# Kernel optimization log

Hardware: AMD Instinct MI355X
Metric: run time of the kernel (lower is better)

Reference implementation:

```python
import jax, jax.numpy as jnp
import numpy as np

NQ = 64
BIG = 1e10

FILTERS = np.array([[1,0,0,1,0,0,1,0,0],
                    [0,0,0,0,0,0,1,1,1],
                    [0,0,1,0,0,1,0,0,1],
                    [1,1,1,0,0,0,0,0,0],
                    [0,0,0,1,0,0,1,1,0],
                    [0,0,0,0,0,1,0,1,1],
                    [0,1,1,0,0,1,0,0,0],
                    [1,1,0,1,0,0,0,0,0]], dtype=np.float32).reshape(8,1,3,3)


def _conv2d(x, k):
    return jax.lax.conv_general_dilated(x, k, (1,1), 'SAME',
                                        dimension_numbers=('NCHW','OIHW','NCHW'))


def _maxpool3(x):  # 3x3 stride-1 maxpool, pad=1 (pads with -inf like torch)
    return jax.lax.reduce_window(x, -jnp.inf, jax.lax.max, (1,1,3,3), (1,1,1,1), 'SAME')


def setup_inputs() -> dict:
    key = jax.random.key(0)
    ks = jax.random.split(key, 5)
    b, h, w = 2, 240, 320
    n = 2 * h * w  # 153600 points
    fx = fy = 300.0
    cx, cy = w / 2.0, h / 2.0
    z  = jax.random.uniform(ks[0], (b, n), minval=1.0, maxval=10.0)
    u  = jax.random.uniform(ks[1], (b, n), minval=0.0, maxval=float(w))
    v  = jax.random.uniform(ks[2], (b, n), minval=0.0, maxval=float(h))
    xw = (u - cx) / fx * z
    yw = (v - cy) / fy * z
    rgb = jax.random.uniform(ks[3], (b, 3, n))
    pp = jnp.concatenate([xw[:, None], yw[:, None], z[:, None],
                          jnp.ones((b, 1, n), jnp.float32), rgb], axis=1)  # [b,7,n]
    conf = jax.random.uniform(ks[4], (b, n))
    pose_w2c = jnp.tile(jnp.eye(4, dtype=jnp.float32)[None], (b, 1, 1))
    K = jnp.tile(jnp.array([[fx, 0, cx], [0, fy, cy], [0, 0, 1.0]], jnp.float32)[None], (b, 1, 1))
    filters = jnp.asarray(FILTERS)
    return {"pp": pp, "conf": conf, "pose_w2c": pose_w2c, "K": K,
            "filters": filters, "h": h, "w": w}


def reference(pp, conf, pose_w2c, K, filters, h, w,
              znear=0.1, zfar=1000.0, conf_thresh=0.0):
    b, _, n = pp.shape
    # world -> camera (wsz=1 so the hi-res pool is identity)
    pc = jnp.einsum('bij,bjn->bin', pose_w2c, pp[:, :4])          # [b,4,n]
    z  = jnp.abs(pc[:, 2])                                        # [b,n]
    xc = pc[:, 0] * K[:, 0, 0][:, None] / z + K[:, 0, 2][:, None]
    yc = pc[:, 1] * K[:, 1, 1][:, None] / z + K[:, 1, 2][:, None]
    x = jnp.round(xc).astype(jnp.int32)
    y = jnp.round(yc).astype(jnp.int32)
    oob = ((x < 0) | (x >= w) | (y < 0) | (y >= h) |
           (z < znear) | (z > zfar) | (conf <= conf_thresh))
    # inverse-depth quantization bounds over valid points only
    inv_lo = 1.0 / jnp.where(oob, 1e-10, z)   # oob -> 1e10, drops out of min
    inv_hi = 1.0 / jnp.where(oob, BIG, z)     # oob -> 1e-10, drops out of max
    dmin = jnp.min(inv_lo, axis=-1, keepdims=True)
    dmax = jnp.max(inv_hi, axis=-1, keepdims=True)
    do = ((inv_hi - dmin) / (dmax - dmin) * (NQ - 1)).astype(jnp.int32)  # [b,n]

    # scatter points into [b, NQ, h, w] z-buffer bins (drop invalid)
    size = b * NQ * h * w
    bidx = jnp.arange(b, dtype=jnp.int32)[:, None]
    idx = ((bidx * NQ + do) * h + y) * w + x
    idx = jnp.where(oob, size, idx).reshape(-1)   # 'size' is out of bounds -> dropped
    zf = z.astype(jnp.float32).reshape(-1)
    dmap = jnp.zeros((size,), jnp.float32).at[idx].set(zf, mode='drop').reshape(b, NQ, h, w)
    cmap = jnp.full((size,), -1.0, jnp.float32).at[idx].set(conf.reshape(-1), mode='drop').reshape(b, NQ, h, w)
    rgb_pts = pp[:, 4:].transpose(0, 2, 1).reshape(-1, 3).astype(jnp.float32)
    rgb = jnp.zeros((size, 3), jnp.float32).at[idx].set(rgb_pts, mode='drop').reshape(b, NQ, h, w, 3)

    # z-buffer composite: nearest non-empty bin per pixel
    dmap = jnp.where(dmap <= 0, BIG, dmap)
    min_idx = jnp.argmin(dmap, axis=1)                             # [b,h,w]
    dflat = jnp.min(dmap, axis=1)
    dflat = jnp.where(dflat >= BIG, 0.0, dflat)
    cflat = jnp.take_along_axis(cmap, min_idx[:, None], axis=1)[:, 0]
    cflat = jnp.maximum(cflat, 0.0)                                # cmap_[cmap_<0]=0
    rflat = jnp.take_along_axis(rgb, min_idx[:, None, :, :, None], axis=1)[:, 0]  # [b,h,w,3]

    # vertical flip (torch.flip over h)
    depths = dflat[:, ::-1][:, None]                               # [b,1,h,w]
    confs  = cflat[:, ::-1][:, None]
    rgbs   = jnp.transpose(rflat[:, ::-1], (0, 3, 1, 2))           # [b,3,h,w]

    # hole filling: 2 iterations of oriented-filter tests + 3x3 max pooling
    ones_k = jnp.ones((1, 1, 3, 3), jnp.float32)
    for _ in range(2):
        tofill = (_conv2d(depths, ones_k) > 0) & (depths <= 0)
        o = _conv2d(depths, filters)                               # [b,8,h,w]
        fill = (jnp.abs(jnp.prod(o, axis=1, keepdims=True)) > 1e-10) & tofill
        f = fill.astype(jnp.float32)
        depths = depths * (1 - f) + f * _maxpool3(depths)
        confs  = confs  * (1 - f) + f * _maxpool3(confs)
        rgbs   = rgbs   * (1 - f) + f * _maxpool3(rgbs)
    return depths, confs, rgbs
```

## Files before the change

kernel.cpp:

```cpp
#include <hip/hip_runtime.h>
#include <stdint.h>

#define NQ 64
#define ZNEAR 0.1f
#define ZFAR 1000.0f
#define FT 16

__device__ __forceinline__ float wave_min_f(float v) {
    #pragma unroll
    for (int off = 1; off < 64; off <<= 1)
        v = fminf(v, __shfl_xor(v, off, 64));
    return v;
}
__device__ __forceinline__ float wave_max_f(float v) {
    #pragma unroll
    for (int off = 1; off < 64; off <<= 1)
        v = fmaxf(v, __shfl_xor(v, off, 64));
    return v;
}

__global__ void k_project(const float* __restrict__ pp, const float* __restrict__ conf,
                          const float* __restrict__ pose, const float* __restrict__ Km,
                          const int* __restrict__ hp, const int* __restrict__ wp,
                          int B, int n,
                          float* __restrict__ zbuf, unsigned* __restrict__ packed,
                          float4* __restrict__ cr4,
                          float* __restrict__ pmin, float* __restrict__ pmax, int nBlk,
                          unsigned* __restrict__ pixwin, int pixTot) {
    int bb = blockIdx.y;
    int i = blockIdx.x * blockDim.x + threadIdx.x;
    size_t ztid = ((size_t)blockIdx.y * gridDim.x + blockIdx.x) * blockDim.x + threadIdx.x;
    if (ztid < (size_t)pixTot) pixwin[ztid] = 0u;

    int h = *hp, w = *wp;
    float inv_lo = INFINITY;
    float inv_hi = 0.0f;
    if (i < n) {
        const float* P  = pose + (size_t)bb * 16;
        const float* km = Km   + (size_t)bb * 9;
        const float* pb = pp   + (size_t)bb * 7 * n;
        float X  = pb[0 * (size_t)n + i];
        float Y  = pb[1 * (size_t)n + i];
        float Z  = pb[2 * (size_t)n + i];
        float Wc = pb[3 * (size_t)n + i];
        float pc0 = P[0] * X + P[1] * Y + P[2]  * Z + P[3]  * Wc;
        float pc1 = P[4] * X + P[5] * Y + P[6]  * Z + P[7]  * Wc;
        float pc2 = P[8] * X + P[9] * Y + P[10] * Z + P[11] * Wc;
        float z = fabsf(pc2);
        float xc = pc0 * km[0] / z + km[2];
        float yc = pc1 * km[4] / z + km[5];
        float xr = rintf(xc);
        float yr = rintf(yc);
        float cf = conf[(size_t)bb * n + i];
        bool valid = (xr >= 0.0f) && (xr <= (float)(w - 1)) &&
                     (yr >= 0.0f) && (yr <= (float)(h - 1)) &&
                     (z >= ZNEAR) && (z <= ZFAR) && (cf > 0.0f);
        unsigned px = valid ? (unsigned)(int)xr : 0u;
        unsigned py = valid ? (unsigned)(int)yr : 0u;
        size_t p = (size_t)bb * n + i;
        zbuf[p] = z;
        packed[p] = (valid ? 0x80000000u : 0u) | px | (py << 12);
        cr4[p] = make_float4(cf, pb[4 * (size_t)n + i], pb[5 * (size_t)n + i], pb[6 * (size_t)n + i]);
        inv_lo = valid ? (1.0f / z) : (1.0f / 1e-10f);
        inv_hi = valid ? (1.0f / z) : (1.0f / 1e10f);
    }
    __shared__ float smin[4], smax[4];
    float wmin = wave_min_f(inv_lo);
    float wmax = wave_max_f(inv_hi);
    int lane = threadIdx.x & 63, wid = threadIdx.x >> 6;
    if (lane == 0) { smin[wid] = wmin; smax[wid] = wmax; }
    __syncthreads();
    if (threadIdx.x == 0) {
        pmin[(size_t)bb * nBlk + blockIdx.x] = fminf(fminf(smin[0], smin[1]), fminf(smin[2], smin[3]));
        pmax[(size_t)bb * nBlk + blockIdx.x] = fmaxf(fmaxf(smax[0], smax[1]), fmaxf(smax[2], smax[3]));
    }
}

__global__ void k_scatter(const float* __restrict__ zbuf, const unsigned* __restrict__ packed,
                          const float* __restrict__ pminb, const float* __restrict__ pmaxb, int nBlk,
                          const int* __restrict__ hp, const int* __restrict__ wp,
                          int B, int n, unsigned* __restrict__ pixwin) {
    __shared__ float smin[4], smax[4];
    __shared__ float sdlo[8], sdhi[8];
    for (int bb = 0; bb < B; ++bb) {
        float lmin = INFINITY, lmax = 0.0f;
        for (int k = threadIdx.x; k < nBlk; k += blockDim.x) {
            lmin = fminf(lmin, pminb[(size_t)bb * nBlk + k]);
            lmax = fmaxf(lmax, pmaxb[(size_t)bb * nBlk + k]);
        }
        lmin = wave_min_f(lmin);
        lmax = wave_max_f(lmax);
        int lane = threadIdx.x & 63, wid = threadIdx.x >> 6;
        if (lane == 0) { smin[wid] = lmin; smax[wid] = lmax; }
        __syncthreads();
        if (threadIdx.x == 0) {
            sdlo[bb] = fminf(fminf(smin[0], smin[1]), fminf(smin[2], smin[3]));
            sdhi[bb] = fmaxf(fmaxf(smax[0], smax[1]), fmaxf(smax[2], smax[3]));
        }
        __syncthreads();
    }
    int p = blockIdx.x * blockDim.x + threadIdx.x;
    if (p >= B * n) return;
    unsigned pk = packed[p];
    if (!(pk & 0x80000000u)) return;
    int bb = p / n;
    int i = p - bb * n;
    float inv = 1.0f / zbuf[p];
    float dlo = sdlo[bb], dhi = sdhi[bb];
    int dq = (int)((inv - dlo) / (dhi - dlo) * (float)(NQ - 1));
    int h = *hp, w = *wp;
    int x = (int)(pk & 0xFFFu);
    int y = (int)((pk >> 12) & 0xFFFu);
    unsigned key = ((unsigned)dq << 20) | (unsigned)(i + 1);
    atomicMax(&pixwin[(size_t)bb * h * w + (size_t)y * w + x], key);
}

__global__ void k_resfill(const float* __restrict__ zbuf, const float4* __restrict__ cr4,
                          const unsigned* __restrict__ pixwin,
                          const float* __restrict__ filt,
                          const int* __restrict__ hp, const int* __restrict__ wp,
                          int B, int n, float* __restrict__ out, int pixTot) {
    int h = *hp, w = *wp;
    int tilesX = (w + FT - 1) / FT;
    int tilesY = (h + FT - 1) / FT;
    int tile = blockIdx.x;
    if (tile >= tilesX * tilesY) return;
    int bb = blockIdx.y;
    int tY = tile / tilesX, tX = tile - tY * tilesX;
    int gy0 = tY * FT - 2, gx0 = tX * FT - 2;
    int hw = h * w;

    __shared__ float s_f[72];
    __shared__ float s_in[5][20][20];
    __shared__ float s_m[5][18][18];
    int tid = threadIdx.x;
    if (tid < 72) s_f[tid] = filt[tid];

    for (int idx = tid; idx < 400; idx += blockDim.x) {
        int yy = idx / 20, xx = idx - yy * 20;
        int gy = gy0 + yy, gx = gx0 + xx;
        float v0 = 0.0f, v1 = 0.0f, v2 = 0.0f, v3 = 0.0f, v4 = 0.0f;
        if (((unsigned)gy < (unsigned)h) && ((unsigned)gx < (unsigned)w)) {
            int ys = h - 1 - gy;
            unsigned key = pixwin[(size_t)bb * hw + (size_t)ys * w + gx];
            if (key) {
                int i = (int)(key & 0xFFFFFu) - 1;
                size_t p = (size_t)bb * n + i;
                v0 = zbuf[p];
                float4 cr = cr4[p];
                v1 = cr.x; v2 = cr.y; v3 = cr.z; v4 = cr.w;
            }
        }
        s_in[0][yy][xx] = v0;
        s_in[1][yy][xx] = v1;
        s_in[2][yy][xx] = v2;
        s_in[3][yy][xx] = v3;
        s_in[4][yy][xx] = v4;
    }
    __syncthreads();

    for (int idx = tid; idx < 324; idx += blockDim.x) {
        int py = idx / 18, px = idx - py * 18;
        int sy = py + 1, sx = px + 1;
        int gy = gy0 + sy, gx = gx0 + sx;
        bool vc = ((unsigned)gy < (unsigned)h) && ((unsigned)gx < (unsigned)w);
        float d[9];
        #pragma unroll
        for (int t = 0; t < 9; ++t) d[t] = s_in[0][sy + t / 3 - 1][sx + t % 3 - 1];
        float s = 0.0f;
        #pragma unroll
        for (int t = 0; t < 9; ++t) s += d[t];
        float dc0 = d[4];
        float ov[5];
        #pragma unroll
        for (int ch = 0; ch < 5; ++ch) ov[ch] = s_in[ch][sy][sx];
        if ((s > 0.0f) && (dc0 <= 0.0f)) {
            float prod = 1.0f;
            #pragma unroll
            for (int k = 0; k < 8; ++k) {
                float o = 0.0f;
                #pragma unroll
                for (int t = 0; t < 9; ++t) o += s_f[k * 9 + t] * d[t];
                prod *= o;
            }
            if (fabsf(prod) > 1e-10f) {
                #pragma unroll
                for (int ch = 0; ch < 5; ++ch) {
                    float m = -INFINITY;
                    #pragma unroll
                    for (int t = 0; t < 9; ++t) {
                        int ny = gy + t / 3 - 1, nx = gx + t % 3 - 1;
                        if (((unsigned)ny < (unsigned)h) && ((unsigned)nx < (unsigned)w))
                            m = fmaxf(m, s_in[ch][sy + t / 3 - 1][sx + t % 3 - 1]);
                    }
                    ov[ch] = m;
                }
            }
        }
        if (!vc) { ov[0] = 0.0f; ov[1] = 0.0f; ov[2] = 0.0f; ov[3] = 0.0f; ov[4] = 0.0f; }
        #pragma unroll
        for (int ch = 0; ch < 5; ++ch) s_m[ch][py][px] = ov[ch];
    }
    __syncthreads();

    int ly = tid >> 4, lx = tid & 15;
    int gy = tY * FT + ly, gx = tX * FT + lx;
    if (((unsigned)gy < (unsigned)h) && ((unsigned)gx < (unsigned)w)) {
        int sy = ly + 1, sx = lx + 1;
        float d[9];
        #pragma unroll
        for (int t = 0; t < 9; ++t) d[t] = s_m[0][sy + t / 3 - 1][sx + t % 3 - 1];
        float s = 0.0f;
        #pragma unroll
        for (int t = 0; t < 9; ++t) s += d[t];
        float dc0 = d[4];
        float ov[5];
        #pragma unroll
        for (int ch = 0; ch < 5; ++ch) ov[ch] = s_m[ch][sy][sx];
        if ((s > 0.0f) && (dc0 <= 0.0f)) {
            float prod = 1.0f;
            #pragma unroll
            for (int k = 0; k < 8; ++k) {
                float o = 0.0f;
                #pragma unroll
                for (int t = 0; t < 9; ++t) o += s_f[k * 9 + t] * d[t];
                prod *= o;
            }
            if (fabsf(prod) > 1e-10f) {
                #pragma unroll
                for (int ch = 0; ch < 5; ++ch) {
                    float m = -INFINITY;
                    #pragma unroll
                    for (int t = 0; t < 9; ++t) {
                        int ny = gy + t / 3 - 1, nx = gx + t % 3 - 1;
                        if (((unsigned)ny < (unsigned)h) && ((unsigned)nx < (unsigned)w))
                            m = fmaxf(m, s_m[ch][sy + t / 3 - 1][sx + t % 3 - 1]);
                    }
                    ov[ch] = m;
                }
            }
        }
        size_t g = (size_t)gy * w + gx;
        out[(size_t)bb * hw + g] = ov[0];
        out[(size_t)pixTot + (size_t)bb * hw + g] = ov[1];
        size_t rb = 2 * (size_t)pixTot;
        out[rb + (((size_t)bb * 3 + 0) * hw) + g] = ov[2];
        out[rb + (((size_t)bb * 3 + 1) * hw) + g] = ov[3];
        out[rb + (((size_t)bb * 3 + 2) * hw) + g] = ov[4];
    }
}

static inline size_t align16(size_t x) { return (x + 15) & ~(size_t)15; }

extern "C" void kernel_launch(void* const* d_in, const int* in_sizes, int n_in,
                              void* d_out, int out_size, void* d_ws, size_t ws_size,
                              hipStream_t stream) {
    const float* pp   = (const float*)d_in[0];
    const float* conf = (const float*)d_in[1];
    const float* pose = (const float*)d_in[2];
    const float* Km   = (const float*)d_in[3];
    const float* filt = (const float*)d_in[4];
    const int*   hp   = (const int*)d_in[5];
    const int*   wp   = (const int*)d_in[6];

    int B = in_sizes[2] / 16;
    int n = in_sizes[1] / B;
    size_t pix = (size_t)out_size / 5;
    size_t npts = (size_t)B * n;
    size_t hw = pix / B;

    const int bs = 256;
    int nBlk = (n + bs - 1) / bs;

    char* ws = (char*)d_ws;
    size_t off = 0;
    unsigned* pixwin = (unsigned*)(ws + off);  off = align16(off + pix * 4);
    float* zbuf   = (float*)(ws + off);        off = align16(off + npts * 4);
    unsigned* packed = (unsigned*)(ws + off);  off = align16(off + npts * 4);
    float4* cr4   = (float4*)(ws + off);       off = align16(off + npts * 16);
    float* pminb  = (float*)(ws + off);        off = align16(off + (size_t)B * nBlk * 4);
    float* pmaxb  = (float*)(ws + off);        off = align16(off + (size_t)B * nBlk * 4);

    float* out = (float*)d_out;
    int pixI = (int)pix;

    dim3 gproj(nBlk, B);
    k_project<<<gproj, bs, 0, stream>>>(pp, conf, pose, Km, hp, wp, B, n,
                                        zbuf, packed, cr4, pminb, pmaxb, nBlk,
                                        pixwin, pixI);

    int nptsI = (int)npts;
    k_scatter<<<(nptsI + bs - 1) / bs, bs, 0, stream>>>(zbuf, packed, pminb, pmaxb, nBlk,
                                                        hp, wp, B, n, pixwin);

    size_t tileBound = hw / (FT * FT) + hw / FT + 2;
    dim3 gfill((unsigned)tileBound, B);
    k_resfill<<<gfill, bs, 0, stream>>>(zbuf, cr4, pixwin, filt, hp, wp, B, n, out, pixI);
}
```

Measured before the change: 105.5 us.

## Fuse projection, scatter and hole-fill into one cooperative persistent kernel

Replaces the three-kernel pipeline (project, scatter, resfill) with a single cooperative kernel that uses grid.sync between phases. Per-batch depth min/max is reduced across blocks in-kernel using unsigned-float atomics in shared memory, and the grid is sized from occupancy times CU count. This removes two kernel launch gaps and the separate reduction, at the cost of grid-wide barriers and a persistent grid that may under-occupy each phase. If the cooperative launch fails, it falls back to the old path.

```diff
diff --git a/kernel.cpp b/kernel.cpp
--- a/kernel.cpp
+++ b/kernel.cpp
@@ -1,10 +1,15 @@
 #include <hip/hip_runtime.h>
+#include <hip/hip_cooperative_groups.h>
 #include <stdint.h>
+
+namespace cg = cooperative_groups;
 
 #define NQ 64
 #define ZNEAR 0.1f
 #define ZFAR 1000.0f
 #define FT 16
+#define BMAX 8
+#define GMAX 2048
 
 __device__ __forceinline__ float wave_min_f(float v) {
     #pragma unroll
@@ -17,6 +22,277 @@
     for (int off = 1; off < 64; off <<= 1)
         v = fmaxf(v, __shfl_xor(v, off, 64));
     return v;
+}
+__device__ __forceinline__ unsigned wave_umin_u(unsigned v) {
+    #pragma unroll
+    for (int off = 1; off < 64; off <<= 1) {
+        unsigned o = (unsigned)__shfl_xor((int)v, off, 64);
+        v = (v < o) ? v : o;
+    }
+    return v;
+}
+__device__ __forceinline__ unsigned wave_umax_u(unsigned v) {
+    #pragma unroll
+    for (int off = 1; off < 64; off <<= 1) {
+        unsigned o = (unsigned)__shfl_xor((int)v, off, 64);
+        v = (v > o) ? v : o;
+    }
+    return v;
+}
+
+__global__ void __launch_bounds__(256, 4)
+k_fused(const float* __restrict__ pp, const float* __restrict__ conf,
+        const float* __restrict__ pose, const float* __restrict__ Km,
+        const float* __restrict__ filt,
+        const int* __restrict__ hp, const int* __restrict__ wp,
+        int B, int n,
+        float* __restrict__ zbuf, unsigned* __restrict__ packed,
+        float4* __restrict__ cr4,
+        unsigned* __restrict__ pminU, unsigned* __restrict__ pmaxU,
+        unsigned* __restrict__ pixwin, float* __restrict__ out)
+{
+    cg::grid_group grid = cg::this_grid();
+    const int h = *hp, w = *wp;
+    const int hw = h * w;
+    const int pixTot = B * hw;
+    const int npts = B * n;
+    const int tid = (int)threadIdx.x;
+    const int gsz = (int)(gridDim.x * blockDim.x);
+    const int gtid = (int)(blockIdx.x * blockDim.x) + tid;
+
+    __shared__ unsigned bmn[BMAX], bmx[BMAX];
+    __shared__ unsigned fw[8];
+    __shared__ float sdlo[BMAX], sdhi[BMAX];
+    __shared__ float s_f[72];
+    __shared__ float s_in[5][20][20];
+    __shared__ float s_m[5][18][18];
+
+    if (tid < BMAX) { bmn[tid] = 0xFFFFFFFFu; bmx[tid] = 0u; }
+    if (tid < 72) s_f[tid] = filt[tid];
+    __syncthreads();
+
+    for (int idx = gtid; idx < pixTot; idx += gsz) pixwin[idx] = 0u;
+
+    int iters = (npts + gsz - 1) / gsz;
+    for (int it = 0; it < iters; ++it) {
+        int p = gtid + it * gsz;
+        bool act = p < npts;
+        int pc = act ? p : (npts - 1);
+        int bb = pc / n;
+        int i = pc - bb * n;
+        unsigned ulo = 0xFFFFFFFFu, uhi = 0u;
+        if (act) {
+            const float* P  = pose + (size_t)bb * 16;
+            const float* km = Km   + (size_t)bb * 9;
+            const float* pb = pp   + (size_t)bb * 7 * n;
+            float X  = pb[0 * (size_t)n + i];
+            float Y  = pb[1 * (size_t)n + i];
+            float Z  = pb[2 * (size_t)n + i];
+            float Wc = pb[3 * (size_t)n + i];
+            float pc0 = P[0] * X + P[1] * Y + P[2]  * Z + P[3]  * Wc;
+            float pc1 = P[4] * X + P[5] * Y + P[6]  * Z + P[7]  * Wc;
+            float pc2 = P[8] * X + P[9] * Y + P[10] * Z + P[11] * Wc;
+            float z = fabsf(pc2);
+            float xc = pc0 * km[0] / z + km[2];
+            float yc = pc1 * km[4] / z + km[5];
+            float xr = rintf(xc);
+            float yr = rintf(yc);
+            float cf = conf[p];
+            bool valid = (xr >= 0.0f) && (xr <= (float)(w - 1)) &&
+                         (yr >= 0.0f) && (yr <= (float)(h - 1)) &&
+                         (z >= ZNEAR) && (z <= ZFAR) && (cf > 0.0f);
+            unsigned px = valid ? (unsigned)(int)xr : 0u;
+            unsigned py = valid ? (unsigned)(int)yr : 0u;
+            zbuf[p] = z;
+            packed[p] = (valid ? 0x80000000u : 0u) | px | (py << 12);
+            cr4[p] = make_float4(cf, pb[4 * (size_t)n + i], pb[5 * (size_t)n + i], pb[6 * (size_t)n + i]);
+            float ilo = valid ? (1.0f / z) : (1.0f / 1e-10f);
+            float ihi = valid ? (1.0f / z) : (1.0f / 1e10f);
+            ulo = __float_as_uint(ilo);
+            uhi = __float_as_uint(ihi);
+        }
+        int bb0 = __shfl(bb, 0, 64);
+        if (__all(bb == bb0)) {
+            unsigned wl = wave_umin_u(ulo);
+            unsigned wh = wave_umax_u(uhi);
+            if ((tid & 63) == 0) { atomicMin(&bmn[bb0], wl); atomicMax(&bmx[bb0], wh); }
+        } else if (act) {
+            atomicMin(&bmn[bb], ulo);
+            atomicMax(&bmx[bb], uhi);
+        }
+    }
+    __syncthreads();
+    if (tid < B) {
+        pminU[(size_t)tid * gridDim.x + blockIdx.x] = bmn[tid];
+        pmaxU[(size_t)tid * gridDim.x + blockIdx.x] = bmx[tid];
+    }
+
+    grid.sync();
+
+    for (int bb = 0; bb < B; ++bb) {
+        unsigned lmin = 0xFFFFFFFFu, lmax = 0u;
+        for (int k = tid; k < (int)gridDim.x; k += (int)blockDim.x) {
+            unsigned a  = pminU[(size_t)bb * gridDim.x + k];
+            unsigned b2 = pmaxU[(size_t)bb * gridDim.x + k];
+            lmin = (lmin < a)  ? lmin : a;
+            lmax = (lmax > b2) ? lmax : b2;
+        }
+        lmin = wave_umin_u(lmin);
+        lmax = wave_umax_u(lmax);
+        int lane = tid & 63, wid = tid >> 6;
+        if (lane == 0) { fw[wid] = lmin; fw[4 + wid] = lmax; }
+        __syncthreads();
+        if (tid == 0) {
+            unsigned m0 = fw[0]; m0 = (m0 < fw[1]) ? m0 : fw[1];
+            m0 = (m0 < fw[2]) ? m0 : fw[2]; m0 = (m0 < fw[3]) ? m0 : fw[3];
+            unsigned m1 = fw[4]; m1 = (m1 > fw[5]) ? m1 : fw[5];
+            m1 = (m1 > fw[6]) ? m1 : fw[6]; m1 = (m1 > fw[7]) ? m1 : fw[7];
+            sdlo[bb] = __uint_as_float(m0);
+            sdhi[bb] = __uint_as_float(m1);
+        }
+        __syncthreads();
+    }
+
+    for (int p = gtid; p < npts; p += gsz) {
+        unsigned pk = packed[p];
+        if (!(pk & 0x80000000u)) continue;
+        int bb = p / n;
+        int i = p - bb * n;
+        float inv = 1.0f / zbuf[p];
+        float dlo = sdlo[bb], dhi = sdhi[bb];
+        int dq = (int)((inv - dlo) / (dhi - dlo) * (float)(NQ - 1));
+        int x = (int)(pk & 0xFFFu);
+        int y = (int)((pk >> 12) & 0xFFFu);
+        unsigned key = ((unsigned)dq << 20) | (unsigned)(i + 1);
+        atomicMax(&pixwin[(size_t)bb * hw + (size_t)y * w + x], key);
+    }
+
+    grid.sync();
+
+    int tilesX = (w + FT - 1) / FT;
+    int tilesY = (h + FT - 1) / FT;
+    int tpb = tilesX * tilesY;
+    int totTiles = B * tpb;
+    for (int t = (int)blockIdx.x; t < totTiles; t += (int)gridDim.x) {
+        int bb = t / tpb;
+        int tile = t - bb * tpb;
+        int tY = tile / tilesX, tX = tile - tY * tilesX;
+        int gy0 = tY * FT - 2, gx0 = tX * FT - 2;
+
+        for (int idx = tid; idx < 400; idx += (int)blockDim.x) {
+            int yy = idx / 20, xx = idx - yy * 20;
+            int gy = gy0 + yy, gx = gx0 + xx;
+            float v0 = 0.0f, v1 = 0.0f, v2 = 0.0f, v3 = 0.0f, v4 = 0.0f;
+            if (((unsigned)gy < (unsigned)h) && ((unsigned)gx < (unsigned)w)) {
+                int ys = h - 1 - gy;
+                unsigned key = pixwin[(size_t)bb * hw + (size_t)ys * w + gx];
+                if (key) {
+                    int i = (int)(key & 0xFFFFFu) - 1;
+                    size_t p = (size_t)bb * n + i;
+                    v0 = zbuf[p];
+                    float4 cr = cr4[p];
+                    v1 = cr.x; v2 = cr.y; v3 = cr.z; v4 = cr.w;
+                }
+            }
+            s_in[0][yy][xx] = v0;
+            s_in[1][yy][xx] = v1;
+            s_in[2][yy][xx] = v2;
+            s_in[3][yy][xx] = v3;
+            s_in[4][yy][xx] = v4;
+        }
+        __syncthreads();
+
+        for (int idx = tid; idx < 324; idx += (int)blockDim.x) {
+            int py = idx / 18, px = idx - py * 18;
+            int sy = py + 1, sx = px + 1;
+            int gy = gy0 + sy, gx = gx0 + sx;
+            bool vc = ((unsigned)gy < (unsigned)h) && ((unsigned)gx < (unsigned)w);
+            float d[9];
+            #pragma unroll
+            for (int tt = 0; tt < 9; ++tt) d[tt] = s_in[0][sy + tt / 3 - 1][sx + tt % 3 - 1];
+            float s = 0.0f;
+            #pragma unroll
+            for (int tt = 0; tt < 9; ++tt) s += d[tt];
+            float dc0 = d[4];
+            float ov[5];
+            #pragma unroll
+            for (int ch = 0; ch < 5; ++ch) ov[ch] = s_in[ch][sy][sx];
+            if ((s > 0.0f) && (dc0 <= 0.0f)) {
+                float prod = 1.0f;
+                #pragma unroll
+                for (int k = 0; k < 8; ++k) {
+                    float o = 0.0f;
+                    #pragma unroll
+                    for (int tt = 0; tt < 9; ++tt) o += s_f[k * 9 + tt] * d[tt];
+                    prod *= o;
+                }
+                if (fabsf(prod) > 1e-10f) {
+                    #pragma unroll
+                    for (int ch = 0; ch < 5; ++ch) {
+                        float m = -INFINITY;
+                        #pragma unroll
+                        for (int tt = 0; tt < 9; ++tt) {
+                            int ny = gy + tt / 3 - 1, nx = gx + tt % 3 - 1;
+                            if (((unsigned)ny < (unsigned)h) && ((unsigned)nx < (unsigned)w))
+                                m = fmaxf(m, s_in[ch][sy + tt / 3 - 1][sx + tt % 3 - 1]);
+                        }
+                        ov[ch] = m;
+                    }
+                }
+            }
+            if (!vc) { ov[0] = 0.0f; ov[1] = 0.0f; ov[2] = 0.0f; ov[3] = 0.0f; ov[4] = 0.0f; }
+            #pragma unroll
+            for (int ch = 0; ch < 5; ++ch) s_m[ch][py][px] = ov[ch];
+        }
+        __syncthreads();
+
+        int ly = tid >> 4, lx = tid & 15;
+        int gy = tY * FT + ly, gx = tX * FT + lx;
+        if (((unsigned)gy < (unsigned)h) && ((unsigned)gx < (unsigned)w)) {
+            int sy = ly + 1, sx = lx + 1;
+            float d[9];
+            #pragma unroll
+            for (int tt = 0; tt < 9; ++tt) d[tt] = s_m[0][sy + tt / 3 - 1][sx + tt % 3 - 1];
+            float s = 0.0f;
+            #pragma unroll
+            for (int tt = 0; tt < 9; ++tt) s += d[tt];
+            float dc0 = d[4];
+            float ov[5];
+            #pragma unroll
+            for (int ch = 0; ch < 5; ++ch) ov[ch] = s_m[ch][sy][sx];
+            if ((s > 0.0f) && (dc0 <= 0.0f)) {
+                float prod = 1.0f;
+                #pragma unroll
+                for (int k = 0; k < 8; ++k) {
+                    float o = 0.0f;
+                    #pragma unroll
+                    for (int tt = 0; tt < 9; ++tt) o += s_f[k * 9 + tt] * d[tt];
+                    prod *= o;
+                }
+                if (fabsf(prod) > 1e-10f) {
+                    #pragma unroll
+                    for (int ch = 0; ch < 5; ++ch) {
+                        float m = -INFINITY;
+                        #pragma unroll
+                        for (int tt = 0; tt < 9; ++tt) {
+                            int ny = gy + tt / 3 - 1, nx = gx + tt % 3 - 1;
+                            if (((unsigned)ny < (unsigned)h) && ((unsigned)nx < (unsigned)w))
+                                m = fmaxf(m, s_m[ch][sy + tt / 3 - 1][sx + tt % 3 - 1]);
+                        }
+                        ov[ch] = m;
+                    }
+                }
+            }
+            size_t g = (size_t)gy * w + gx;
+            out[(size_t)bb * hw + g] = ov[0];
+            out[(size_t)pixTot + (size_t)bb * hw + g] = ov[1];
+            size_t rb = 2 * (size_t)pixTot;
+            out[rb + (((size_t)bb * 3 + 0) * hw) + g] = ov[2];
+            out[rb + (((size_t)bb * 3 + 1) * hw) + g] = ov[3];
+            out[rb + (((size_t)bb * 3 + 2) * hw) + g] = ov[4];
+        }
+        __syncthreads();
+    }
 }
 
 __global__ void k_project(const float* __restrict__ pp, const float* __restrict__ conf,
@@ -267,7 +543,6 @@
     int n = in_sizes[1] / B;
     size_t pix = (size_t)out_size / 5;
     size_t npts = (size_t)B * n;
-    size_t hw = pix / B;
 
     const int bs = 256;
     int nBlk = (n + bs - 1) / bs;
@@ -278,11 +553,41 @@
     float* zbuf   = (float*)(ws + off);        off = align16(off + npts * 4);
     unsigned* packed = (unsigned*)(ws + off);  off = align16(off + npts * 4);
     float4* cr4   = (float4*)(ws + off);       off = align16(off + npts * 16);
-    float* pminb  = (float*)(ws + off);        off = align16(off + (size_t)B * nBlk * 4);
-    float* pmaxb  = (float*)(ws + off);        off = align16(off + (size_t)B * nBlk * 4);
+    unsigned* pminU = (unsigned*)(ws + off);   off = align16(off + (size_t)GMAX * BMAX * 4);
+    unsigned* pmaxU = (unsigned*)(ws + off);   off = align16(off + (size_t)GMAX * BMAX * 4);
 
     float* out = (float*)d_out;
     int pixI = (int)pix;
+
+    static int G = 0;
+    if (G == 0) {
+        int nb = 0;
+        if (hipOccupancyMaxActiveBlocksPerMultiprocessor(&nb, k_fused, bs, 0) != hipSuccess || nb < 1)
+            nb = 2;
+        int dev = 0;
+        hipGetDevice(&dev);
+        int cus = 0;
+        if (hipDeviceGetAttribute(&cus, hipDeviceAttributeMultiprocessorCount, dev) != hipSuccess || cus < 1)
+            cus = 256;
+        long long g = (long long)nb * cus;
+        if (g > GMAX) g = GMAX;
+        if (g < 64) g = 64;
+        G = (int)g;
+    }
+
+    {
+        void* kargs[] = { (void*)&pp, (void*)&conf, (void*)&pose, (void*)&Km, (void*)&filt,
+                          (void*)&hp, (void*)&wp, (void*)&B, (void*)&n,
+                          (void*)&zbuf, (void*)&packed, (void*)&cr4,
+                          (void*)&pminU, (void*)&pmaxU, (void*)&pixwin, (void*)&out };
+        hipError_t e = hipLaunchCooperativeKernel((const void*)k_fused, dim3((unsigned)G), dim3(bs),
+                                                  kargs, 0, stream);
+        if (e == hipSuccess) return;
+    }
+
+    float* pminb = (float*)pminU;
+    float* pmaxb = (float*)pmaxU;
+    size_t hw = pix / B;
 
     dim3 gproj(nBlk, B);
     k_project<<<gproj, bs, 0, stream>>>(pp, conf, pose, Km, hp, wp, B, n,
```

After: 225.8 us. 2.14x slower.

## Pack depth into 64-bit winner key and grid-stride fill tiles

Applied to the files above, without the earlier changes.

The per-pixel winner key becomes 64 bits, with the point's depth bits in the low word, so the fill kernel reads depth straight from the key instead of gathering from zbuf. Projection writes a single interleaved uint2 (packed coords plus z) in place of two separate arrays, and the scatter kernel does one 8-byte load. The fill kernel changes from one block per tile with a loose tile bound to a persistent grid-stride loop over tiles with a capped grid. In exchange the atomics and the pixel buffer double in width, and each tile iteration now needs an extra barrier.

```diff
diff --git a/kernel.cpp b/kernel.cpp
--- a/kernel.cpp
+++ b/kernel.cpp
@@ -23,14 +23,13 @@
                           const float* __restrict__ pose, const float* __restrict__ Km,
                           const int* __restrict__ hp, const int* __restrict__ wp,
                           int B, int n,
-                          float* __restrict__ zbuf, unsigned* __restrict__ packed,
-                          float4* __restrict__ cr4,
+                          uint2* __restrict__ pz, float4* __restrict__ cr4,
                           float* __restrict__ pmin, float* __restrict__ pmax, int nBlk,
-                          unsigned* __restrict__ pixwin, int pixTot) {
+                          unsigned long long* __restrict__ pixwin, int pixTot) {
     int bb = blockIdx.y;
     int i = blockIdx.x * blockDim.x + threadIdx.x;
     size_t ztid = ((size_t)blockIdx.y * gridDim.x + blockIdx.x) * blockDim.x + threadIdx.x;
-    if (ztid < (size_t)pixTot) pixwin[ztid] = 0u;
+    if (ztid < (size_t)pixTot) pixwin[ztid] = 0ull;
 
     int h = *hp, w = *wp;
     float inv_lo = INFINITY;
@@ -58,8 +57,7 @@
         unsigned px = valid ? (unsigned)(int)xr : 0u;
         unsigned py = valid ? (unsigned)(int)yr : 0u;
         size_t p = (size_t)bb * n + i;
-        zbuf[p] = z;
-        packed[p] = (valid ? 0x80000000u : 0u) | px | (py << 12);
+        pz[p] = make_uint2((valid ? 0x80000000u : 0u) | px | (py << 12), __float_as_uint(z));
         cr4[p] = make_float4(cf, pb[4 * (size_t)n + i], pb[5 * (size_t)n + i], pb[6 * (size_t)n + i]);
         inv_lo = valid ? (1.0f / z) : (1.0f / 1e-10f);
         inv_hi = valid ? (1.0f / z) : (1.0f / 1e10f);
@@ -76,10 +74,10 @@
     }
 }
 
-__global__ void k_scatter(const float* __restrict__ zbuf, const unsigned* __restrict__ packed,
+__global__ void k_scatter(const uint2* __restrict__ pz,
                           const float* __restrict__ pminb, const float* __restrict__ pmaxb, int nBlk,
                           const int* __restrict__ hp, const int* __restrict__ wp,
-                          int B, int n, unsigned* __restrict__ pixwin) {
+                          int B, int n, unsigned long long* __restrict__ pixwin) {
     __shared__ float smin[4], smax[4];
     __shared__ float sdlo[8], sdhi[8];
     for (int bb = 0; bb < B; ++bb) {
@@ -101,152 +99,160 @@
     }
     int p = blockIdx.x * blockDim.x + threadIdx.x;
     if (p >= B * n) return;
-    unsigned pk = packed[p];
+    uint2 v = pz[p];
+    unsigned pk = v.x;
     if (!(pk & 0x80000000u)) return;
     int bb = p / n;
     int i = p - bb * n;
-    float inv = 1.0f / zbuf[p];
+    float z = __uint_as_float(v.y);
+    float inv = 1.0f / z;
     float dlo = sdlo[bb], dhi = sdhi[bb];
     int dq = (int)((inv - dlo) / (dhi - dlo) * (float)(NQ - 1));
     int h = *hp, w = *wp;
     int x = (int)(pk & 0xFFFu);
     int y = (int)((pk >> 12) & 0xFFFu);
-    unsigned key = ((unsigned)dq << 20) | (unsigned)(i + 1);
+    unsigned key32 = ((unsigned)dq << 20) | (unsigned)(i + 1);
+    unsigned long long key = ((unsigned long long)key32 << 32) | (unsigned long long)v.y;
     atomicMax(&pixwin[(size_t)bb * h * w + (size_t)y * w + x], key);
 }
 
-__global__ void k_resfill(const float* __restrict__ zbuf, const float4* __restrict__ cr4,
-                          const unsigned* __restrict__ pixwin,
+__global__ void k_resfill(const float4* __restrict__ cr4,
+                          const unsigned long long* __restrict__ pixwin,
                           const float* __restrict__ filt,
                           const int* __restrict__ hp, const int* __restrict__ wp,
                           int B, int n, float* __restrict__ out, int pixTot) {
     int h = *hp, w = *wp;
+    int hw = h * w;
     int tilesX = (w + FT - 1) / FT;
     int tilesY = (h + FT - 1) / FT;
-    int tile = blockIdx.x;
-    if (tile >= tilesX * tilesY) return;
-    int bb = blockIdx.y;
-    int tY = tile / tilesX, tX = tile - tY * tilesX;
-    int gy0 = tY * FT - 2, gx0 = tX * FT - 2;
-    int hw = h * w;
+    int tpb = tilesX * tilesY;
+    int totTiles = B * tpb;
+    int tid = threadIdx.x;
 
     __shared__ float s_f[72];
     __shared__ float s_in[5][20][20];
     __shared__ float s_m[5][18][18];
-    int tid = threadIdx.x;
     if (tid < 72) s_f[tid] = filt[tid];
 
-    for (int idx = tid; idx < 400; idx += blockDim.x) {
-        int yy = idx / 20, xx = idx - yy * 20;
-        int gy = gy0 + yy, gx = gx0 + xx;
-        float v0 = 0.0f, v1 = 0.0f, v2 = 0.0f, v3 = 0.0f, v4 = 0.0f;
+    for (int t = (int)blockIdx.x; t < totTiles; t += (int)gridDim.x) {
+        int bb = t / tpb;
+        int tile = t - bb * tpb;
+        int tY = tile / tilesX, tX = tile - tY * tilesX;
+        int gy0 = tY * FT - 2, gx0 = tX * FT - 2;
+
+        for (int idx = tid; idx < 400; idx += (int)blockDim.x) {
+            int yy = idx / 20, xx = idx - yy * 20;
+            int gy = gy0 + yy, gx = gx0 + xx;
+            float v0 = 0.0f, v1 = 0.0f, v2 = 0.0f, v3 = 0.0f, v4 = 0.0f;
+            if (((unsigned)gy < (unsigned)h) && ((unsigned)gx < (unsigned)w)) {
+                int ys = h - 1 - gy;
+                unsigned long long key = pixwin[(size_t)bb * hw + (size_t)ys * w + gx];
+                if (key) {
+                    int i = (int)((unsigned)(key >> 32) & 0xFFFFFu) - 1;
+                    size_t p = (size_t)bb * n + i;
+                    v0 = __uint_as_float((unsigned)(key & 0xFFFFFFFFull));
+                    float4 cr = cr4[p];
+                    v1 = cr.x; v2 = cr.y; v3 = cr.z; v4 = cr.w;
+                }
+            }
+            s_in[0][yy][xx] = v0;
+            s_in[1][yy][xx] = v1;
+            s_in[2][yy][xx] = v2;
+            s_in[3][yy][xx] = v3;
+            s_in[4][yy][xx] = v4;
+        }
+        __syncthreads();
+
+        for (int idx = tid; idx < 324; idx += (int)blockDim.x) {
+            int py = idx / 18, px = idx - py * 18;
+            int sy = py + 1, sx = px + 1;
+            int gy = gy0 + sy, gx = gx0 + sx;
+            bool vc = ((unsigned)gy < (unsigned)h) && ((unsigned)gx < (unsigned)w);
+            float d[9];
+            #pragma unroll
+            for (int tt = 0; tt < 9; ++tt) d[tt] = s_in[0][sy + tt / 3 - 1][sx + tt % 3 - 1];
+            float s = 0.0f;
+            #pragma unroll
+            for (int tt = 0; tt < 9; ++tt) s += d[tt];
+            float dc0 = d[4];
+            float ov[5];
+            #pragma unroll
+            for (int ch = 0; ch < 5; ++ch) ov[ch] = s_in[ch][sy][sx];
+            if ((s > 0.0f) && (dc0 <= 0.0f)) {
+                float prod = 1.0f;
+                #pragma unroll
+                for (int k = 0; k < 8; ++k) {
+                    float o = 0.0f;
+                    #pragma unroll
+                    for (int tt = 0; tt < 9; ++tt) o += s_f[k * 9 + tt] * d[tt];
+                    prod *= o;
+                }
+                if (fabsf(prod) > 1e-10f) {
+                    #pragma unroll
+                    for (int ch = 0; ch < 5; ++ch) {
+                        float m = -INFINITY;
+                        #pragma unroll
+                        for (int tt = 0; tt < 9; ++tt) {
+                            int ny = gy + tt / 3 - 1, nx = gx + tt % 3 - 1;
+                            if (((unsigned)ny < (unsigned)h) && ((unsigned)nx < (unsigned)w))
+                                m = fmaxf(m, s_in[ch][sy + tt / 3 - 1][sx + tt % 3 - 1]);
+                        }
+                        ov[ch] = m;
+                    }
+                }
+            }
+            if (!vc) { ov[0] = 0.0f; ov[1] = 0.0f; ov[2] = 0.0f; ov[3] = 0.0f; ov[4] = 0.0f; }
+            #pragma unroll
+            for (int ch = 0; ch < 5; ++ch) s_m[ch][py][px] = ov[ch];
+        }
+        __syncthreads();
+
+        int ly = tid >> 4, lx = tid & 15;
+        int gy = tY * FT + ly, gx = tX * FT + lx;
         if (((unsigned)gy < (unsigned)h) && ((unsigned)gx < (unsigned)w)) {
-            int ys = h - 1 - gy;
-            unsigned key = pixwin[(size_t)bb * hw + (size_t)ys * w + gx];
-            if (key) {
-                int i = (int)(key & 0xFFFFFu) - 1;
-                size_t p = (size_t)bb * n + i;
-                v0 = zbuf[p];
-                float4 cr = cr4[p];
-                v1 = cr.x; v2 = cr.y; v3 = cr.z; v4 = cr.w;
+            int sy = ly + 1, sx = lx + 1;
+            float d[9];
+            #pragma unroll
+            for (int tt = 0; tt < 9; ++tt) d[tt] = s_m[0][sy + tt / 3 - 1][sx + tt % 3 - 1];
+            float s = 0.0f;
+            #pragma unroll
+            for (int tt = 0; tt < 9; ++tt) s += d[tt];
+            float dc0 = d[4];
+            float ov[5];
+            #pragma unroll
+            for (int ch = 0; ch < 5; ++ch) ov[ch] = s_m[ch][sy][sx];
+            if ((s > 0.0f) && (dc0 <= 0.0f)) {
+                float prod = 1.0f;
+                #pragma unroll
+                for (int k = 0; k < 8; ++k) {
+                    float o = 0.0f;
+                    #pragma unroll
+                    for (int tt = 0; tt < 9; ++tt) o += s_f[k * 9 + tt] * d[tt];
+                    prod *= o;
+                }
+                if (fabsf(prod) > 1e-10f) {
+                    #pragma unroll
+                    for (int ch = 0; ch < 5; ++ch) {
+                        float m = -INFINITY;
+                        #pragma unroll
+                        for (int tt = 0; tt < 9; ++tt) {
+                            int ny = gy + tt / 3 - 1, nx = gx + tt % 3 - 1;
+                            if (((unsigned)ny < (unsigned)h) && ((unsigned)nx < (unsigned)w))
+                                m = fmaxf(m, s_m[ch][sy + tt / 3 - 1][sx + tt % 3 - 1]);
+                        }
+                        ov[ch] = m;
+                    }
+                }
             }
-        }
-        s_in[0][yy][xx] = v0;
-        s_in[1][yy][xx] = v1;
-        s_in[2][yy][xx] = v2;
-        s_in[3][yy][xx] = v3;
-        s_in[4][yy][xx] = v4;
-    }
-    __syncthreads();
-
-    for (int idx = tid; idx < 324; idx += blockDim.x) {
-        int py = idx / 18, px = idx - py * 18;
-        int sy = py + 1, sx = px + 1;
-        int gy = gy0 + sy, gx = gx0 + sx;
-        bool vc = ((unsigned)gy < (unsigned)h) && ((unsigned)gx < (unsigned)w);
-        float d[9];
-        #pragma unroll
-        for (int t = 0; t < 9; ++t) d[t] = s_in[0][sy + t / 3 - 1][sx + t % 3 - 1];
-        float s = 0.0f;
-        #pragma unroll
-        for (int t = 0; t < 9; ++t) s += d[t];
-        float dc0 = d[4];
-        float ov[5];
-        #pragma unroll
-        for (int ch = 0; ch < 5; ++ch) ov[ch] = s_in[ch][sy][sx];
-        if ((s > 0.0f) && (dc0 <= 0.0f)) {
-            float prod = 1.0f;
-            #pragma unroll
-            for (int k = 0; k < 8; ++k) {
-                float o = 0.0f;
-                #pragma unroll
-                for (int t = 0; t < 9; ++t) o += s_f[k * 9 + t] * d[t];
-                prod *= o;
-            }
-            if (fabsf(prod) > 1e-10f) {
-                #pragma unroll
-                for (int ch = 0; ch < 5; ++ch) {
-                    float m = -INFINITY;
-                    #pragma unroll
-                    for (int t = 0; t < 9; ++t) {
-                        int ny = gy + t / 3 - 1, nx = gx + t % 3 - 1;
-                        if (((unsigned)ny < (unsigned)h) && ((unsigned)nx < (unsigned)w))
-                            m = fmaxf(m, s_in[ch][sy + t / 3 - 1][sx + t % 3 - 1]);
-                    }
-                    ov[ch] = m;
-                }
-            }
-        }
-        if (!vc) { ov[0] = 0.0f; ov[1] = 0.0f; ov[2] = 0.0f; ov[3] = 0.0f; ov[4] = 0.0f; }
-        #pragma unroll
-        for (int ch = 0; ch < 5; ++ch) s_m[ch][py][px] = ov[ch];
-    }
-    __syncthreads();
-
-    int ly = tid >> 4, lx = tid & 15;
-    int gy = tY * FT + ly, gx = tX * FT + lx;
-    if (((unsigned)gy < (unsigned)h) && ((unsigned)gx < (unsigned)w)) {
-        int sy = ly + 1, sx = lx + 1;
-        float d[9];
-        #pragma unroll
-        for (int t = 0; t < 9; ++t) d[t] = s_m[0][sy + t / 3 - 1][sx + t % 3 - 1];
-        float s = 0.0f;
-        #pragma unroll
-        for (int t = 0; t < 9; ++t) s += d[t];
-        float dc0 = d[4];
-        float ov[5];
-        #pragma unroll
-        for (int ch = 0; ch < 5; ++ch) ov[ch] = s_m[ch][sy][sx];
-        if ((s > 0.0f) && (dc0 <= 0.0f)) {
-            float prod = 1.0f;
-            #pragma unroll
-            for (int k = 0; k < 8; ++k) {
-                float o = 0.0f;
-                #pragma unroll
-                for (int t = 0; t < 9; ++t) o += s_f[k * 9 + t] * d[t];
-                prod *= o;
-            }
-            if (fabsf(prod) > 1e-10f) {
-                #pragma unroll
-                for (int ch = 0; ch < 5; ++ch) {
-                    float m = -INFINITY;
-                    #pragma unroll
-                    for (int t = 0; t < 9; ++t) {
-                        int ny = gy + t / 3 - 1, nx = gx + t % 3 - 1;
-                        if (((unsigned)ny < (unsigned)h) && ((unsigned)nx < (unsigned)w))
-                            m = fmaxf(m, s_m[ch][sy + t / 3 - 1][sx + t % 3 - 1]);
-                    }
-                    ov[ch] = m;
-                }
-            }
-        }
-        size_t g = (size_t)gy * w + gx;
-        out[(size_t)bb * hw + g] = ov[0];
-        out[(size_t)pixTot + (size_t)bb * hw + g] = ov[1];
-        size_t rb = 2 * (size_t)pixTot;
-        out[rb + (((size_t)bb * 3 + 0) * hw) + g] = ov[2];
-        out[rb + (((size_t)bb * 3 + 1) * hw) + g] = ov[3];
-        out[rb + (((size_t)bb * 3 + 2) * hw) + g] = ov[4];
+            size_t g = (size_t)gy * w + gx;
+            out[(size_t)bb * hw + g] = ov[0];
+            out[(size_t)pixTot + (size_t)bb * hw + g] = ov[1];
+            size_t rb = 2 * (size_t)pixTot;
+            out[rb + (((size_t)bb * 3 + 0) * hw) + g] = ov[2];
+            out[rb + (((size_t)bb * 3 + 1) * hw) + g] = ov[3];
+            out[rb + (((size_t)bb * 3 + 2) * hw) + g] = ov[4];
+        }
+        __syncthreads();
     }
 }
 
@@ -274,9 +280,8 @@
 
     char* ws = (char*)d_ws;
     size_t off = 0;
-    unsigned* pixwin = (unsigned*)(ws + off);  off = align16(off + pix * 4);
-    float* zbuf   = (float*)(ws + off);        off = align16(off + npts * 4);
-    unsigned* packed = (unsigned*)(ws + off);  off = align16(off + npts * 4);
+    unsigned long long* pixwin = (unsigned long long*)(ws + off);  off = align16(off + pix * 8);
+    uint2* pz     = (uint2*)(ws + off);        off = align16(off + npts * 8);
     float4* cr4   = (float4*)(ws + off);       off = align16(off + npts * 16);
     float* pminb  = (float*)(ws + off);        off = align16(off + (size_t)B * nBlk * 4);
     float* pmaxb  = (float*)(ws + off);        off = align16(off + (size_t)B * nBlk * 4);
@@ -286,14 +291,15 @@
 
     dim3 gproj(nBlk, B);
     k_project<<<gproj, bs, 0, stream>>>(pp, conf, pose, Km, hp, wp, B, n,
-                                        zbuf, packed, cr4, pminb, pmaxb, nBlk,
+                                        pz, cr4, pminb, pmaxb, nBlk,
                                         pixwin, pixI);
 
     int nptsI = (int)npts;
-    k_scatter<<<(nptsI + bs - 1) / bs, bs, 0, stream>>>(zbuf, packed, pminb, pmaxb, nBlk,
+    k_scatter<<<(nptsI + bs - 1) / bs, bs, 0, stream>>>(pz, pminb, pmaxb, nBlk,
                                                         hp, wp, B, n, pixwin);
 
-    size_t tileBound = hw / (FT * FT) + hw / FT + 2;
-    dim3 gfill((unsigned)tileBound, B);
-    k_resfill<<<gfill, bs, 0, stream>>>(zbuf, cr4, pixwin, filt, hp, wp, B, n, out, pixI);
-}
+    long long G = (long long)B * (long long)(hw / (FT * FT)) + 128;
+    if (G > 2048) G = 2048;
+    if (G < 64) G = 64;
+    k_resfill<<<dim3((unsigned)G), bs, 0, stream>>>(cr4, pixwin, filt, hp, wp, B, n, out, pixI);
+}
```

Result: faster. 102.1 us (-3.2%).
